# Optimization experiments

Hardware: AMD Instinct MI355X
Metric: run time of the kernel (lower is better)

Reference implementation:

```python
import jax, jax.numpy as jnp
import numpy as np

B, S, D, E, K = 4, 4096, 2048, 64, 2
LN_EPS = 1e-5
TEMP_EPS = 1e-6
Z_LOSS_COEF = 0.001
LB_COEF = 0.1


def setup_inputs() -> dict:
    key = jax.random.key(0)
    k1, k2 = jax.random.split(key)
    x = jax.random.normal(k1, (B, S, D), dtype=jnp.float32)
    # kaiming_normal fan_in (std = 1/sqrt(D)) scaled by 0.01, as in __init__
    W = jax.random.normal(k2, (E, D), dtype=jnp.float32) * jnp.float32(0.01 / np.sqrt(D))
    gamma = jnp.ones((E,), jnp.float32)   # LayerNorm weight
    beta = jnp.zeros((E,), jnp.float32)   # LayerNorm bias
    temperature = jnp.full((1,), 0.5, jnp.float32)
    return {"x": x, "W": W, "gamma": gamma, "beta": beta, "temperature": temperature}


def reference(x, W, gamma, beta, temperature):
    b, s, d = x.shape
    xf = x.reshape(-1, d)                                  # [N, D]
    logits = xf @ W.T                                      # [N, E]
    # LayerNorm over expert dim (biased variance, eps=1e-5, matches torch)
    mu = logits.mean(axis=-1, keepdims=True)
    var = jnp.mean(jnp.square(logits - mu), axis=-1, keepdims=True)
    logits = (logits - mu) * jax.lax.rsqrt(var + LN_EPS) * gamma + beta
    # temperature-scaled softmax
    routing_weights = jax.nn.softmax(logits / (temperature + TEMP_EPS), axis=-1)  # [N, E]
    # top-k + scatter into dense dispatch mask
    top_w, top_idx = jax.lax.top_k(routing_weights, K)     # [N, K]
    n = routing_weights.shape[0]
    dispatch = jnp.zeros_like(routing_weights).at[jnp.arange(n)[:, None], top_idx].set(top_w)
    dispatch = dispatch.reshape(b, s, E)                   # [B, S, E]
    # aux losses
    expert_load = dispatch.mean(axis=1)                    # [B, E]
    load_balance_loss = jnp.std(expert_load, ddof=1) / expert_load.mean() * 10.0
    router_z_loss = jnp.mean(jnp.square(logits))
    total_loss = ZLC * router_z_loss + LB_COEF * load_balance_loss if False else (
        Z_LOSS_COEF * router_z_loss + LB_COEF * load_balance_loss)
    return jax.lax.stop_gradient(routing_weights), dispatch, total_loss
```

## Files before the change

### kernel.cpp

```cpp
#include <hip/hip_runtime.h>
#include <hip/hip_bf16.h>
#include <float.h>
#include <math.h>

#define B_DIM 4
#define S_DIM 4096
#define D_DIM 2048
#define E_DIM 64
#define N_TOK 16384
#define TOKS 32
#define NBLK (N_TOK / TOKS)
#define NTHR 512
#define BK 64
#define SLICES 4
#define DSLICE (D_DIM / SLICES)
#define KSTEPS (DSLICE / BK)
#define GAP_THRESH 1e-3f
#define MAXFLAG 16

typedef __bf16 bf16x8_t __attribute__((ext_vector_type(8)));
typedef float f32x4_t __attribute__((ext_vector_type(4)));

union U8 { bf16x8_t v; unsigned short u[8]; };

__device__ __forceinline__ void split2(float f, unsigned short& h, unsigned short& l) {
    unsigned int u = __float_as_uint(f);
    h = (unsigned short)(u >> 16);
    float hf = __uint_as_float(u & 0xFFFF0000u);
    l = (unsigned short)(__float_as_uint(f - hf) >> 16);
}

__global__ void wsplit(const float* __restrict__ W, unsigned short* __restrict__ wh,
                       unsigned short* __restrict__ wl, float* __restrict__ wshdr) {
    const int i = blockIdx.x * 256 + threadIdx.x;
    if (blockIdx.x == 0) { wshdr[threadIdx.x] = 0.f; wshdr[threadIdx.x + 256] = 0.f; }
    float4 v = *(const float4*)(W + (size_t)i * 4);
    ushort4 h, l;
    split2(v.x, h.x, l.x); split2(v.y, h.y, l.y);
    split2(v.z, h.z, l.z); split2(v.w, h.w, l.w);
    *(ushort4*)(wh + (size_t)i * 4) = h;
    *(ushort4*)(wl + (size_t)i * 4) = l;
}

__global__ __launch_bounds__(NTHR, 4) void router_main(
    const float* __restrict__ x, const float* __restrict__ W,
    const unsigned short* __restrict__ whg, const unsigned short* __restrict__ wlg,
    const float* __restrict__ gamma, const float* __restrict__ beta,
    const float* __restrict__ temperature,
    float* __restrict__ out_rw, float* __restrict__ out_dp,
    float* __restrict__ g_zsum, float* __restrict__ g_load)
{
    __shared__ float part[SLICES][TOKS][E_DIM + 2];
    __shared__ float lgt[TOKS][E_DIM + 1];
    __shared__ float lgm[E_DIM], lbt[E_DIM], loadsum[E_DIM];
    __shared__ float smu[TOKS], srs[TOKS], sinv[TOKS];
    __shared__ int sel1[TOKS], sel2[TOKS];
    __shared__ int ftok[MAXFLAG], fcand[MAXFLAG][3];
    __shared__ int nflag;

    const int tid = threadIdx.x;
    const int tokBase = blockIdx.x * TOKS;
    const int lane = tid & 63;
    const int wv = tid >> 6;
    const int g  = wv & 1;
    const int sl = wv >> 1;
    const int l15 = lane & 15;
    const int quad = lane >> 4;

    if (tid == 0) nflag = 0;
    if (tid < E_DIM) { lgm[tid] = gamma[tid]; lbt[tid] = beta[tid]; loadsum[tid] = 0.f; }

    const float* xp = x + (size_t)(tokBase + g * 16 + l15) * D_DIM + sl * DSLICE + quad * 8;

    const unsigned short* wb[4][2];
    {
        const size_t lanepos = (size_t)l15 * D_DIM + sl * DSLICE + quad * 8;
        #pragma unroll
        for (int t = 0; t < 4; ++t) {
            wb[t][0] = whg + lanepos + (size_t)t * 16 * D_DIM;
            wb[t][1] = wlg + lanepos + (size_t)t * 16 * D_DIM;
        }
    }

    f32x4_t acc[4];
    #pragma unroll
    for (int t = 0; t < 4; ++t) acc[t] = (f32x4_t){0.f, 0.f, 0.f, 0.f};

    float4 xq[4], xn[4];
    #pragma unroll
    for (int c = 0; c < 2; ++c) {
        xq[c * 2]     = *(const float4*)(xp + c * 32);
        xq[c * 2 + 1] = *(const float4*)(xp + c * 32 + 4);
    }

    for (int s = 0; s < KSTEPS; ++s) {
        const bool more = (s + 1 < KSTEPS);
        if (more) {
            const float* xg = xp + (s + 1) * BK;
            #pragma unroll
            for (int c = 0; c < 2; ++c) {
                xn[c * 2]     = *(const float4*)(xg + c * 32);
                xn[c * 2 + 1] = *(const float4*)(xg + c * 32 + 4);
            }
        }
        #pragma unroll
        for (int h = 0; h < 2; ++h) {
            bf16x8_t bh[4], bl[4];
            #pragma unroll
            for (int t = 0; t < 4; ++t) {
                bh[t] = *(const bf16x8_t*)(wb[t][0] + s * BK + h * 32);
                bl[t] = *(const bf16x8_t*)(wb[t][1] + s * BK + h * 32);
            }
            float tf[8] = {xq[h*2].x, xq[h*2].y, xq[h*2].z, xq[h*2].w,
                           xq[h*2+1].x, xq[h*2+1].y, xq[h*2+1].z, xq[h*2+1].w};
            U8 ah, al;
            #pragma unroll
            for (int k = 0; k < 8; ++k) split2(tf[k], ah.u[k], al.u[k]);
            #pragma unroll
            for (int t = 0; t < 4; ++t) {
                acc[t] = __builtin_amdgcn_mfma_f32_16x16x32_bf16(ah.v, bh[t], acc[t], 0, 0, 0);
                acc[t] = __builtin_amdgcn_mfma_f32_16x16x32_bf16(ah.v, bl[t], acc[t], 0, 0, 0);
                acc[t] = __builtin_amdgcn_mfma_f32_16x16x32_bf16(al.v, bh[t], acc[t], 0, 0, 0);
            }
        }
        if (more) {
            #pragma unroll
            for (int j = 0; j < 4; ++j) xq[j] = xn[j];
        }
    }

    #pragma unroll
    for (int t = 0; t < 4; ++t)
        #pragma unroll
        for (int r = 0; r < 4; ++r)
            part[sl][g * 16 + quad * 4 + r][t * 16 + l15] = acc[t][r];
    __syncthreads();

    for (int i = tid; i < TOKS * E_DIM; i += NTHR) {
        int r = i >> 6, c = i & 63;
        lgt[r][c] = (part[0][r][c] + part[1][r][c]) + (part[2][r][c] + part[3][r][c]);
    }
    __syncthreads();

    if (wv < 2) {
        const int tok = wv * 16 + l15;
        const int q = quad;
        const float it = 1.f / (temperature[0] + 1e-6f);
        float s1 = 0.f, s2 = 0.f;
        #pragma unroll
        for (int e = 0; e < 16; ++e) { float v = lgt[tok][q * 16 + e]; s1 += v; s2 += v * v; }
        s1 += __shfl_xor(s1, 16); s1 += __shfl_xor(s1, 32);
        s2 += __shfl_xor(s2, 16); s2 += __shfl_xor(s2, 32);
        const float mu  = s1 * (1.f / 64.f);
        const float var = s2 * (1.f / 64.f) - mu * mu;
        const float rs  = rsqrtf(var + 1e-5f);
        if (q == 0) { smu[tok] = mu; srs[tok] = rs; }

        float m0 = -FLT_MAX, m1 = -FLT_MAX, m2 = -FLT_MAX;
        int   i0 = -1, i1 = -1, i2 = -1;
        float zl = 0.f;
        #pragma unroll
        for (int e = 0; e < 16; ++e) {
            int c = q * 16 + e;
            float y = (lgt[tok][c] - mu) * rs * lgm[c] + lbt[c];
            lgt[tok][c] = y;
            zl += y * y;
            if (y > m0)      { m2 = m1; i2 = i1; m1 = m0; i1 = i0; m0 = y; i0 = c; }
            else if (y > m1) { m2 = m1; i2 = i1; m1 = y; i1 = c; }
            else if (y > m2) { m2 = y; i2 = c; }
        }
        #pragma unroll
        for (int d = 16; d <= 32; d <<= 1) {
            float n0 = __shfl_xor(m0, d), n1 = __shfl_xor(m1, d), n2 = __shfl_xor(m2, d);
            int   j0 = __shfl_xor(i0, d), j1 = __shfl_xor(i1, d), j2 = __shfl_xor(i2, d);
            bool t0 = (m0 > n0) || (m0 == n0 && i0 < j0);
            float r0v = t0 ? m0 : n0; int r0i = t0 ? i0 : j0;
            float A0v = t0 ? m1 : m0; int A0i = t0 ? i1 : i0;
            float A1v = t0 ? m2 : m1; int A1i = t0 ? i2 : i1;
            float B0v = t0 ? n0 : n1; int B0i = t0 ? j0 : j1;
            float B1v = t0 ? n1 : n2; int B1i = t0 ? j1 : j2;
            bool t1 = (A0v > B0v) || (A0v == B0v && A0i < B0i);
            float r1v = t1 ? A0v : B0v; int r1i = t1 ? A0i : B0i;
            float A0w = t1 ? A1v : A0v; int A0j = t1 ? A1i : A0i;
            float B0w = t1 ? B0v : B1v; int B0j = t1 ? B0i : B1i;
            bool t2 = (A0w > B0w) || (A0w == B0w && A0j < B0j);
            float r2v = t2 ? A0w : B0w; int r2i = t2 ? A0j : B0j;
            m0 = r0v; i0 = r0i; m1 = r1v; i1 = r1i; m2 = r2v; i2 = r2i;
        }
        if (q == 0) {
            sel1[tok] = i0; sel2[tok] = i1;
            if (m1 - m2 < GAP_THRESH) {
                int sf = atomicAdd(&nflag, 1);
                if (sf < MAXFLAG) { ftok[sf] = tok; fcand[sf][0] = i0; fcand[sf][1] = i1; fcand[sf][2] = i2; }
            }
        }
        float es = 0.f;
        #pragma unroll
        for (int e = 0; e < 16; ++e) {
            int c = q * 16 + e;
            float ev = __expf((lgt[tok][c] - m0) * it);
            lgt[tok][c] = ev; es += ev;
        }
        es += __shfl_xor(es, 16); es += __shfl_xor(es, 32);
        if (q == 0) sinv[tok] = 1.f / es;
        zl += __shfl_xor(zl, 1); zl += __shfl_xor(zl, 2); zl += __shfl_xor(zl, 4);
        zl += __shfl_xor(zl, 8); zl += __shfl_xor(zl, 16); zl += __shfl_xor(zl, 32);
        if (lane == 0) atomicAdd(g_zsum, zl);
    }
    __syncthreads();

    const int nf = min(nflag, MAXFLAG);
    for (int f = wv; f < nf; f += 8) {
        const int tk = ftok[f];
        const int c0 = fcand[f][0], c1 = fcand[f][1], c2 = fcand[f][2];
        const float* xr = x + (size_t)(tokBase + tk) * D_DIM;
        const float* w0 = W + (size_t)c0 * D_DIM;
        const float* w1 = W + (size_t)c1 * D_DIM;
        const float* w2 = W + (size_t)c2 * D_DIM;
        double L0 = 0.0, L1 = 0.0, L2 = 0.0;
        for (int i = lane; i < D_DIM; i += 64) {
            double xv = (double)xr[i];
            L0 += xv * (double)w0[i];
            L1 += xv * (double)w1[i];
            L2 += xv * (double)w2[i];
        }
        #pragma unroll
        for (int off = 32; off; off >>= 1) {
            L0 += __shfl_down(L0, off);
            L1 += __shfl_down(L1, off);
            L2 += __shfl_down(L2, off);
        }
        if (lane == 0) {
            double dmu = (double)smu[tk], drs = (double)srs[tk];
            double y0 = (L0 - dmu) * drs * (double)lgm[c0] + (double)lbt[c0];
            double y1 = (L1 - dmu) * drs * (double)lgm[c1] + (double)lbt[c1];
            double y2 = (L2 - dmu) * drs * (double)lgm[c2] + (double)lbt[c2];
            bool g01 = (y0 > y1) || (y0 == y1 && c0 < c1);
            bool g02 = (y0 > y2) || (y0 == y2 && c0 < c2);
            bool g12 = (y1 > y2) || (y1 == y2 && c1 < c2);
            int a, b;
            if (!g01 && !g02)      { a = c1; b = c2; }
            else if (g01 && !g12)  { a = c0; b = c2; }
            else                   { a = c0; b = c1; }
            sel1[tk] = a; sel2[tk] = b;
        }
    }
    __syncthreads();

    if (tid < TOKS) {
        float inv = sinv[tid];
        atomicAdd(&loadsum[sel1[tid]], lgt[tid][sel1[tid]] * inv);
        atomicAdd(&loadsum[sel2[tid]], lgt[tid][sel2[tid]] * inv);
    }
    __syncthreads();
    if (tid < E_DIM) atomicAdd(&g_load[(tokBase >> 12) * E_DIM + tid], loadsum[tid]);

    float* orw = out_rw + (size_t)tokBase * E_DIM;
    float* odp = out_dp + (size_t)tokBase * E_DIM;
    for (int i = tid; i < TOKS * E_DIM; i += NTHR) {
        int r = i >> 6, c = i & 63;
        float p = lgt[r][c] * sinv[r];
        orw[i] = p;
        odp[i] = (c == sel1[r] || c == sel2[r]) ? p : 0.f;
    }
}

__global__ void router_fin(const float* __restrict__ ws, float* __restrict__ out_loss) {
    __shared__ float sv[B_DIM * E_DIM];
    const int tid = threadIdx.x;
    sv[tid] = ws[8 + tid] * (1.f / S_DIM);
    __syncthreads();
    if (tid == 0) {
        float s = 0.f;
        for (int i = 0; i < B_DIM * E_DIM; ++i) s += sv[i];
        const float mean = s * (1.f / (B_DIM * E_DIM));
        float ss = 0.f;
        for (int i = 0; i < B_DIM * E_DIM; ++i) { float d = sv[i] - mean; ss += d * d; }
        const float sd = sqrtf(ss * (1.f / (B_DIM * E_DIM - 1)));
        const float z = ws[0] * (1.f / ((float)N_TOK * E_DIM));
        out_loss[0] = 0.001f * z + 0.1f * (sd / mean) * 10.f;
    }
}

extern "C" void kernel_launch(void* const* d_in, const int* in_sizes, int n_in,
                              void* d_out, int out_size, void* d_ws, size_t ws_size,
                              hipStream_t stream) {
    const float* x     = (const float*)d_in[0];
    const float* W     = (const float*)d_in[1];
    const float* gamma = (const float*)d_in[2];
    const float* beta  = (const float*)d_in[3];
    const float* temp  = (const float*)d_in[4];
    float* out  = (float*)d_out;
    float* rw   = out;
    float* dp   = out + (size_t)N_TOK * E_DIM;
    float* loss = out + 2 * (size_t)N_TOK * E_DIM;
    float* ws   = (float*)d_ws;

    unsigned short* whg = (unsigned short*)((char*)d_ws + 4096);
    unsigned short* wlg = whg + (size_t)E_DIM * D_DIM;

    wsplit<<<dim3(128), dim3(256), 0, stream>>>(W, whg, wlg, ws);
    router_main<<<dim3(NBLK), dim3(NTHR), 0, stream>>>(x, W, whg, wlg, gamma, beta, temp,
                                                       rw, dp, ws, ws + 8);
    router_fin<<<dim3(1), dim3(256), 0, stream>>>(ws, loss);
}
```

Baseline: 261.6 us.

## Prepack split weights into MFMA fragment order and fold loss finalize into main kernel

The weight split kernel now writes the bf16 hi/lo halves in a layout ordered by slice, k-step, half, tile and lane. Each wave's B-fragment loads therefore become contiguous coalesced 16-byte reads instead of strided rows, and all eight fragments for a k-step are loaded up front. The separate finalize kernel is removed. The last block, found with an atomic counter and threadfence, computes the loss, which saves one launch but adds a fence and atomic per block.

Measured after the change: 327.6 us. +25.2%, slower.

```diff
diff --git a/kernel.cpp b/kernel.cpp
--- a/kernel.cpp
+++ b/kernel.cpp
@@ -34,12 +34,27 @@
                        unsigned short* __restrict__ wl, float* __restrict__ wshdr) {
     const int i = blockIdx.x * 256 + threadIdx.x;
     if (blockIdx.x == 0) { wshdr[threadIdx.x] = 0.f; wshdr[threadIdx.x + 256] = 0.f; }
-    float4 v = *(const float4*)(W + (size_t)i * 4);
-    ushort4 h, l;
-    split2(v.x, h.x, l.x); split2(v.y, h.y, l.y);
-    split2(v.z, h.z, l.z); split2(v.w, h.w, l.w);
-    *(ushort4*)(wh + (size_t)i * 4) = h;
-    *(ushort4*)(wl + (size_t)i * 4) = l;
+    const int e    = i >> 8;
+    const int k8   = i & 255;
+    const int quad = k8 & 3;
+    const int h    = (k8 >> 2) & 1;
+    const int s    = (k8 >> 3) & 7;
+    const int sl   = k8 >> 6;
+    const int t    = e >> 4;
+    const int l15  = e & 15;
+    const int lane = quad * 16 + l15;
+    const size_t f = ((size_t)((sl * 8 + s) * 2 + h) * 4 + t) * 64 + lane;
+    float4 a = *(const float4*)(W + (size_t)e * D_DIM + k8 * 8);
+    float4 b = *(const float4*)(W + (size_t)e * D_DIM + k8 * 8 + 4);
+    ushort4 h0, l0, h1, l1;
+    split2(a.x, h0.x, l0.x); split2(a.y, h0.y, l0.y);
+    split2(a.z, h0.z, l0.z); split2(a.w, h0.w, l0.w);
+    split2(b.x, h1.x, l1.x); split2(b.y, h1.y, l1.y);
+    split2(b.z, h1.z, l1.z); split2(b.w, h1.w, l1.w);
+    *(ushort4*)(wh + f * 8)     = h0;
+    *(ushort4*)(wh + f * 8 + 4) = h1;
+    *(ushort4*)(wl + f * 8)     = l0;
+    *(ushort4*)(wl + f * 8 + 4) = l1;
 }
 
 __global__ __launch_bounds__(NTHR, 4) void router_main(
@@ -48,7 +63,8 @@
     const float* __restrict__ gamma, const float* __restrict__ beta,
     const float* __restrict__ temperature,
     float* __restrict__ out_rw, float* __restrict__ out_dp,
-    float* __restrict__ g_zsum, float* __restrict__ g_load)
+    float* __restrict__ g_zsum, float* __restrict__ g_load,
+    float* __restrict__ out_loss)
 {
     __shared__ float part[SLICES][TOKS][E_DIM + 2];
     __shared__ float lgt[TOKS][E_DIM + 1];
@@ -57,6 +73,8 @@
     __shared__ int sel1[TOKS], sel2[TOKS];
     __shared__ int ftok[MAXFLAG], fcand[MAXFLAG][3];
     __shared__ int nflag;
+    __shared__ int lastflag;
+    __shared__ float sv[B_DIM * E_DIM];
 
     const int tid = threadIdx.x;
     const int tokBase = blockIdx.x * TOKS;
@@ -72,15 +90,8 @@
 
     const float* xp = x + (size_t)(tokBase + g * 16 + l15) * D_DIM + sl * DSLICE + quad * 8;
 
-    const unsigned short* wb[4][2];
-    {
-        const size_t lanepos = (size_t)l15 * D_DIM + sl * DSLICE + quad * 8;
-        #pragma unroll
-        for (int t = 0; t < 4; ++t) {
-            wb[t][0] = whg + lanepos + (size_t)t * 16 * D_DIM;
-            wb[t][1] = wlg + lanepos + (size_t)t * 16 * D_DIM;
-        }
-    }
+    const unsigned short* whb = whg + (size_t)sl * 32768 + lane * 8;
+    const unsigned short* wlb = wlg + (size_t)sl * 32768 + lane * 8;
 
     f32x4_t acc[4];
     #pragma unroll
@@ -95,6 +106,19 @@
 
     for (int s = 0; s < KSTEPS; ++s) {
         const bool more = (s + 1 < KSTEPS);
+        const unsigned short* hb = whb + s * 4096;
+        const unsigned short* lb = wlb + s * 4096;
+        bf16x8_t BH0[4], BL0[4], BH1[4], BL1[4];
+        #pragma unroll
+        for (int t = 0; t < 4; ++t) {
+            BH0[t] = *(const bf16x8_t*)(hb + t * 512);
+            BL0[t] = *(const bf16x8_t*)(lb + t * 512);
+        }
+        #pragma unroll
+        for (int t = 0; t < 4; ++t) {
+            BH1[t] = *(const bf16x8_t*)(hb + 2048 + t * 512);
+            BL1[t] = *(const bf16x8_t*)(lb + 2048 + t * 512);
+        }
         if (more) {
             const float* xg = xp + (s + 1) * BK;
             #pragma unroll
@@ -103,24 +127,30 @@
                 xn[c * 2 + 1] = *(const float4*)(xg + c * 32 + 4);
             }
         }
-        #pragma unroll
-        for (int h = 0; h < 2; ++h) {
-            bf16x8_t bh[4], bl[4];
+        {
+            float tf[8] = {xq[0].x, xq[0].y, xq[0].z, xq[0].w,
+                           xq[1].x, xq[1].y, xq[1].z, xq[1].w};
+            U8 ah, al;
+            #pragma unroll
+            for (int k = 0; k < 8; ++k) split2(tf[k], ah.u[k], al.u[k]);
             #pragma unroll
             for (int t = 0; t < 4; ++t) {
-                bh[t] = *(const bf16x8_t*)(wb[t][0] + s * BK + h * 32);
-                bl[t] = *(const bf16x8_t*)(wb[t][1] + s * BK + h * 32);
+                acc[t] = __builtin_amdgcn_mfma_f32_16x16x32_bf16(ah.v, BH0[t], acc[t], 0, 0, 0);
+                acc[t] = __builtin_amdgcn_mfma_f32_16x16x32_bf16(ah.v, BL0[t], acc[t], 0, 0, 0);
+                acc[t] = __builtin_amdgcn_mfma_f32_16x16x32_bf16(al.v, BH0[t], acc[t], 0, 0, 0);
             }
-            float tf[8] = {xq[h*2].x, xq[h*2].y, xq[h*2].z, xq[h*2].w,
-                           xq[h*2+1].x, xq[h*2+1].y, xq[h*2+1].z, xq[h*2+1].w};
+        }
+        {
+            float tf[8] = {xq[2].x, xq[2].y, xq[2].z, xq[2].w,
+                           xq[3].x, xq[3].y, xq[3].z, xq[3].w};
             U8 ah, al;
             #pragma unroll
             for (int k = 0; k < 8; ++k) split2(tf[k], ah.u[k], al.u[k]);
             #pragma unroll
             for (int t = 0; t < 4; ++t) {
-                acc[t] = __builtin_amdgcn_mfma_f32_16x16x32_bf16(ah.v, bh[t], acc[t], 0, 0, 0);
-                acc[t] = __builtin_amdgcn_mfma_f32_16x16x32_bf16(ah.v, bl[t], acc[t], 0, 0, 0);
-                acc[t] = __builtin_amdgcn_mfma_f32_16x16x32_bf16(al.v, bh[t], acc[t], 0, 0, 0);
+                acc[t] = __builtin_amdgcn_mfma_f32_16x16x32_bf16(ah.v, BH1[t], acc[t], 0, 0, 0);
+                acc[t] = __builtin_amdgcn_mfma_f32_16x16x32_bf16(ah.v, BL1[t], acc[t], 0, 0, 0);
+                acc[t] = __builtin_amdgcn_mfma_f32_16x16x32_bf16(al.v, BH1[t], acc[t], 0, 0, 0);
             }
         }
         if (more) {
@@ -263,22 +293,28 @@
         orw[i] = p;
         odp[i] = (c == sel1[r] || c == sel2[r]) ? p : 0.f;
     }
-}
-
-__global__ void router_fin(const float* __restrict__ ws, float* __restrict__ out_loss) {
-    __shared__ float sv[B_DIM * E_DIM];
-    const int tid = threadIdx.x;
-    sv[tid] = ws[8 + tid] * (1.f / S_DIM);
-    __syncthreads();
+
+    __threadfence();
     if (tid == 0) {
-        float s = 0.f;
-        for (int i = 0; i < B_DIM * E_DIM; ++i) s += sv[i];
-        const float mean = s * (1.f / (B_DIM * E_DIM));
-        float ss = 0.f;
-        for (int i = 0; i < B_DIM * E_DIM; ++i) { float d = sv[i] - mean; ss += d * d; }
-        const float sd = sqrtf(ss * (1.f / (B_DIM * E_DIM - 1)));
-        const float z = ws[0] * (1.f / ((float)N_TOK * E_DIM));
-        out_loss[0] = 0.001f * z + 0.1f * (sd / mean) * 10.f;
+        int prev = atomicAdd((int*)(g_zsum + 4), 1);
+        lastflag = (prev == NBLK - 1);
+    }
+    __syncthreads();
+    if (lastflag) {
+        __threadfence();
+        if (tid < B_DIM * E_DIM)
+            sv[tid] = atomicAdd(&g_load[tid], 0.f) * (1.f / S_DIM);
+        __syncthreads();
+        if (tid == 0) {
+            float s = 0.f;
+            for (int i = 0; i < B_DIM * E_DIM; ++i) s += sv[i];
+            const float mean = s * (1.f / (B_DIM * E_DIM));
+            float ss = 0.f;
+            for (int i = 0; i < B_DIM * E_DIM; ++i) { float d = sv[i] - mean; ss += d * d; }
+            const float sd = sqrtf(ss * (1.f / (B_DIM * E_DIM - 1)));
+            const float z = atomicAdd(g_zsum, 0.f) * (1.f / ((float)N_TOK * E_DIM));
+            out_loss[0] = 0.001f * z + 0.1f * (sd / mean) * 10.f;
+        }
     }
 }
 
@@ -299,8 +335,7 @@
     unsigned short* whg = (unsigned short*)((char*)d_ws + 4096);
     unsigned short* wlg = whg + (size_t)E_DIM * D_DIM;
 
-    wsplit<<<dim3(128), dim3(256), 0, stream>>>(W, whg, wlg, ws);
+    wsplit<<<dim3(64), dim3(256), 0, stream>>>(W, whg, wlg, ws);
     router_main<<<dim3(NBLK), dim3(NTHR), 0, stream>>>(x, W, whg, wlg, gamma, beta, temp,
-                                                       rw, dp, ws, ws + 8);
-    router_fin<<<dim3(1), dim3(256), 0, stream>>>(ws, loss);
+                                                       rw, dp, ws, ws + 8, loss);
 }
```

## Stage pre-swizzled W hi/lo tiles through LDS with register double-buffering

Applied to the files above, without the earlier changes.

The W split kernel now writes the hi/lo bf16 halves in an MFMA-fragment-ordered layout. The main kernel loads them cooperatively with fully coalesced 16-byte loads into a 64KB LDS arena that is reused for the partial-sum buffers. Each k-step prefetches the next W tile into registers and writes it to LDS between two barriers, replacing the old strided per-lane global W loads. The cost is a 64KB LDS footprint, which may limit occupancy against the 4-blocks launch bound, plus extra barriers per step.

After: 287.1 us. 9.8% more time.

```diff
diff --git a/kernel.cpp b/kernel.cpp
--- a/kernel.cpp
+++ b/kernel.cpp
@@ -34,12 +34,27 @@
                        unsigned short* __restrict__ wl, float* __restrict__ wshdr) {
     const int i = blockIdx.x * 256 + threadIdx.x;
     if (blockIdx.x == 0) { wshdr[threadIdx.x] = 0.f; wshdr[threadIdx.x + 256] = 0.f; }
-    float4 v = *(const float4*)(W + (size_t)i * 4);
-    ushort4 h, l;
-    split2(v.x, h.x, l.x); split2(v.y, h.y, l.y);
-    split2(v.z, h.z, l.z); split2(v.w, h.w, l.w);
-    *(ushort4*)(wh + (size_t)i * 4) = h;
-    *(ushort4*)(wl + (size_t)i * 4) = l;
+    const int e    = i >> 8;
+    const int k8   = i & 255;
+    const int quad = k8 & 3;
+    const int h    = (k8 >> 2) & 1;
+    const int s    = (k8 >> 3) & 7;
+    const int sl   = k8 >> 6;
+    const int t    = e >> 4;
+    const int l15  = e & 15;
+    const int lane = quad * 16 + l15;
+    const size_t f = ((size_t)((sl * 8 + s) * 2 + h) * 4 + t) * 64 + lane;
+    float4 a = *(const float4*)(W + (size_t)e * D_DIM + k8 * 8);
+    float4 b = *(const float4*)(W + (size_t)e * D_DIM + k8 * 8 + 4);
+    ushort4 h0, l0, h1, l1;
+    split2(a.x, h0.x, l0.x); split2(a.y, h0.y, l0.y);
+    split2(a.z, h0.z, l0.z); split2(a.w, h0.w, l0.w);
+    split2(b.x, h1.x, l1.x); split2(b.y, h1.y, l1.y);
+    split2(b.z, h1.z, l1.z); split2(b.w, h1.w, l1.w);
+    *(ushort4*)(wh + f * 8)     = h0;
+    *(ushort4*)(wh + f * 8 + 4) = h1;
+    *(ushort4*)(wl + f * 8)     = l0;
+    *(ushort4*)(wl + f * 8 + 4) = l1;
 }
 
 __global__ __launch_bounds__(NTHR, 4) void router_main(
@@ -50,8 +65,12 @@
     float* __restrict__ out_rw, float* __restrict__ out_dp,
     float* __restrict__ g_zsum, float* __restrict__ g_load)
 {
-    __shared__ float part[SLICES][TOKS][E_DIM + 2];
-    __shared__ float lgt[TOKS][E_DIM + 1];
+    __shared__ __align__(16) unsigned char arena[65536];
+    unsigned short* const wbufH = (unsigned short*)arena;
+    unsigned short* const wbufL = (unsigned short*)(arena + 32768);
+    float (* const part)[TOKS][E_DIM + 2] = (float (*)[TOKS][E_DIM + 2])arena;
+    float (* const lgt)[E_DIM + 1] = (float (*)[E_DIM + 1])(arena + 33792);
+
     __shared__ float lgm[E_DIM], lbt[E_DIM], loadsum[E_DIM];
     __shared__ float smu[TOKS], srs[TOKS], sinv[TOKS];
     __shared__ int sel1[TOKS], sel2[TOKS];
@@ -72,30 +91,40 @@
 
     const float* xp = x + (size_t)(tokBase + g * 16 + l15) * D_DIM + sl * DSLICE + quad * 8;
 
-    const unsigned short* wb[4][2];
-    {
-        const size_t lanepos = (size_t)l15 * D_DIM + sl * DSLICE + quad * 8;
-        #pragma unroll
-        for (int t = 0; t < 4; ++t) {
-            wb[t][0] = whg + lanepos + (size_t)t * 16 * D_DIM;
-            wb[t][1] = wlg + lanepos + (size_t)t * 16 * D_DIM;
-        }
-    }
+    const unsigned short* whsrc = whg + tid * 8;
+    const unsigned short* wlsrc = wlg + tid * 8;
 
     f32x4_t acc[4];
     #pragma unroll
     for (int t = 0; t < 4; ++t) acc[t] = (f32x4_t){0.f, 0.f, 0.f, 0.f};
 
     float4 xq[4], xn[4];
+    #pragma unroll
+    for (int k = 0; k < SLICES; ++k) {
+        uint4 vh = *(const uint4*)(whsrc + k * 32768);
+        uint4 vl = *(const uint4*)(wlsrc + k * 32768);
+        *(uint4*)(wbufH + k * 4096 + tid * 8) = vh;
+        *(uint4*)(wbufL + k * 4096 + tid * 8) = vl;
+    }
     #pragma unroll
     for (int c = 0; c < 2; ++c) {
         xq[c * 2]     = *(const float4*)(xp + c * 32);
         xq[c * 2 + 1] = *(const float4*)(xp + c * 32 + 4);
     }
+    __syncthreads();
+
+    const unsigned short* hb = wbufH + sl * 4096;
+    const unsigned short* lb = wbufL + sl * 4096;
 
     for (int s = 0; s < KSTEPS; ++s) {
         const bool more = (s + 1 < KSTEPS);
+        uint4 wrh[4], wrl[4];
         if (more) {
+            #pragma unroll
+            for (int k = 0; k < SLICES; ++k) {
+                wrh[k] = *(const uint4*)(whsrc + k * 32768 + (s + 1) * 4096);
+                wrl[k] = *(const uint4*)(wlsrc + k * 32768 + (s + 1) * 4096);
+            }
             const float* xg = xp + (s + 1) * BK;
             #pragma unroll
             for (int c = 0; c < 2; ++c) {
@@ -108,8 +137,8 @@
             bf16x8_t bh[4], bl[4];
             #pragma unroll
             for (int t = 0; t < 4; ++t) {
-                bh[t] = *(const bf16x8_t*)(wb[t][0] + s * BK + h * 32);
-                bl[t] = *(const bf16x8_t*)(wb[t][1] + s * BK + h * 32);
+                bh[t] = *(const bf16x8_t*)(hb + (h * 4 + t) * 512 + lane * 8);
+                bl[t] = *(const bf16x8_t*)(lb + (h * 4 + t) * 512 + lane * 8);
             }
             float tf[8] = {xq[h*2].x, xq[h*2].y, xq[h*2].z, xq[h*2].w,
                            xq[h*2+1].x, xq[h*2+1].y, xq[h*2+1].z, xq[h*2+1].w};
@@ -123,9 +152,16 @@
                 acc[t] = __builtin_amdgcn_mfma_f32_16x16x32_bf16(al.v, bh[t], acc[t], 0, 0, 0);
             }
         }
+        __syncthreads();
         if (more) {
             #pragma unroll
+            for (int k = 0; k < SLICES; ++k) {
+                *(uint4*)(wbufH + k * 4096 + tid * 8) = wrh[k];
+                *(uint4*)(wbufL + k * 4096 + tid * 8) = wrl[k];
+            }
+            #pragma unroll
             for (int j = 0; j < 4; ++j) xq[j] = xn[j];
+            __syncthreads();
         }
     }
 
@@ -299,7 +335,7 @@
     unsigned short* whg = (unsigned short*)((char*)d_ws + 4096);
     unsigned short* wlg = whg + (size_t)E_DIM * D_DIM;
 
-    wsplit<<<dim3(128), dim3(256), 0, stream>>>(W, whg, wlg, ws);
+    wsplit<<<dim3(64), dim3(256), 0, stream>>>(W, whg, wlg, ws);
     router_main<<<dim3(NBLK), dim3(NTHR), 0, stream>>>(x, W, whg, wlg, gamma, beta, temp,
                                                        rw, dp, ws, ws + 8);
     router_fin<<<dim3(1), dim3(256), 0, stream>>>(ws, loss);
```
